# Optimization experiments

Hardware: AMD Instinct MI355X
Metric: run time of the kernel (lower is better)

Reference implementation:

```python
import jax, jax.numpy as jnp
import numpy as np

B, T, D, H, W = 2, 16, 64, 64, 64
E, EXP = 4, 2
TWO_D = 2 * D
HID = EXP * TWO_D


def layernorm(x, g, b, eps=1e-5):
    m = x.mean(-1, keepdims=True)
    v = ((x - m) ** 2).mean(-1, keepdims=True)
    return (x - m) / jnp.sqrt(v + eps) * g + b


def pscan(A, X):
    # h_t = A_t * h_{t-1} + X_t, scanned over axis=1 (time); complex-valued.
    def comb(c1, c2):
        a1, x1 = c1
        a2, x2 = c2
        return a1 * a2, a2 * x1 + x2
    return jax.lax.associative_scan(comb, (A, X), axis=1)[1]


def setup_inputs() -> dict:
    key = jax.random.key(0)
    ks = jax.random.split(key, 24)
    def s(i, shape, scale=0.05):
        return jax.random.normal(ks[i], shape, jnp.float32) * scale
    return {
        "x_re": jax.random.normal(ks[0], (B, T, D, H, W), jnp.float32),
        "x_im": jax.random.normal(ks[1], (B, T, D, H, W), jnp.float32),
        "dt": jax.random.uniform(ks[2], (T,), jnp.float32, 0.5, 1.5),
        "ln_s_g": jnp.ones((TWO_D,), jnp.float32),
        "ln_s_b": jnp.zeros((TWO_D,), jnp.float32),
        "conv_w": s(3, (TWO_D, TWO_D, 3, 3)),
        "conv_b": jnp.zeros((TWO_D,), jnp.float32),
        "ln_t_g": jnp.ones((TWO_D,), jnp.float32),
        "ln_t_b": jnp.zeros((TWO_D,), jnp.float32),
        "enc_re": s(4, (D, D)), "enc_im": s(5, (D, D)),
        "dec_re": s(6, (D, D)), "dec_im": s(7, (D, D)),
        "alpha": s(8, (D,), 0.5), "omega": s(9, (D,), 1.0),
        "wg": s(10, (TWO_D, D)), "bg": jnp.zeros((D,), jnp.float32),
        "p_re": s(11, (D, D)), "p_im": s(12, (D, D)),
        "w_drift": s(13, (TWO_D, D)), "b_drift": jnp.zeros((D,), jnp.float32),
        "w_router": s(14, (TWO_D, E)),
        "w1": s(15, (E, TWO_D, HID)), "w2": s(16, (E, HID, TWO_D)),
        "noise_scale": jnp.float32(0.01),
    }


def reference(x_re, x_im, dt, ln_s_g, ln_s_b, conv_w, conv_b, ln_t_g, ln_t_b,
              enc_re, enc_im, dec_re, dec_im, alpha, omega, wg, bg,
              p_re, p_im, w_drift, b_drift, w_router, w1, w2, noise_scale):
    x = x_re + 1j * x_im  # [B,T,D,H,W] complex64
    N = B * T
    xf = x.reshape(N, D, H, W)
    xr = jnp.concatenate([xf.real, xf.imag], axis=1)  # [N,2D,H,W]
    # spatial LayerNorm over channels
    xn = layernorm(xr.transpose(0, 2, 3, 1), ln_s_g, ln_s_b).transpose(0, 3, 1, 2)
    # Clifford spatial conv (standard 3x3 same-conv on stacked re/im channels)
    xs = jax.lax.conv_general_dilated(xn, conv_w, (1, 1), 'SAME',
                                      dimension_numbers=('NCHW', 'OIHW', 'NCHW'))
    xs = xs + conv_b[None, :, None, None]
    x_sc = xs[:, :D] + 1j * xs[:, D:]            # [N,D,H,W]
    x5 = x_sc.reshape(B, T, D, H, W)              # complex
    # basis encode: complex channel mixing
    enc = enc_re + 1j * enc_im
    u_t = jnp.einsum('bthwd,de->bthwe', x5.transpose(0, 1, 3, 4, 2), enc)  # [B,T,H,W,D]

    # ---- global flux tracker (pscan #1) ----
    x_mean = x5.mean(axis=(-2, -1))               # [B,T,D] complex
    feat = jnp.concatenate([x_mean.real, x_mean.imag], axis=-1)  # [B,T,2D]
    gate = jax.nn.sigmoid(feat @ wg + bg)         # [B,T,D]
    flux_A = gate.astype(jnp.complex64)
    flux_X = (1.0 - gate) * x_mean
    flux_state = pscan(flux_A, flux_X)            # [B,T,D]
    flux_out = flux_state @ (p_re + 1j * p_im)    # [B,T,D]
    drift_in = jnp.concatenate([flux_out.real, flux_out.imag], axis=-1)
    drift = drift_in @ w_drift + b_drift          # [B,T,D] (dead code in source; kept for fidelity)
    drift_c = drift[..., : D // 2] + 1j * drift[..., D // 2:]
    del drift_c

    # ---- temporal propagation (pscan #2) ----
    dt_e = dt.reshape(1, T, 1, 1, 1)              # broadcast (B,T,H,W,1)
    lam = -jax.nn.softplus(alpha) + 1j * omega    # [D]
    decay = jnp.exp(lam * dt_e)                   # [1,T,1,1,D]
    forcing = (decay - 1.0) / lam                 # ZOH forcing operator
    u_scaled = u_t * forcing                      # [B,T,H,W,D]
    decay_full = jnp.broadcast_to(decay, (B, T, H, W, D))
    A_time = decay_full.transpose(0, 2, 3, 1, 4).reshape(B * H * W, T, D)
    X_time = u_scaled.transpose(0, 2, 3, 1, 4).reshape(B * H * W, T, D)
    Y = pscan(A_time, X_time)
    u_out = Y.reshape(B, H, W, T, D).transpose(0, 3, 1, 2, 4)  # [B,T,H,W,D]
    # deterministic surrogate for the SDE stochastic term (state-proportional)
    u_out = u_out + noise_scale * jnp.sqrt(dt_e) * u_out
    dec = dec_re + 1j * dec_im
    x_out = jnp.einsum('bthwd,de->bthwe', u_out, dec)  # decode
    x_out = x_out.transpose(0, 1, 4, 2, 3).reshape(N, D, H, W)
    xo_r = jnp.concatenate([x_out.real, x_out.imag], axis=1)
    xo_n = layernorm(xo_r.transpose(0, 2, 3, 1), ln_t_g, ln_t_b)  # [N,H,W,2D]

    # ---- MoE FFN over pixels (soft mixture of experts) ----
    gates = jax.nn.softmax(xo_n @ w_router, axis=-1)  # [N,H,W,E]
    acc = jnp.zeros_like(xo_n)
    for e in range(E):
        h = jax.nn.gelu(xo_n @ w1[e])
        acc = acc + gates[..., e:e + 1] * (h @ w2[e])
    delta = acc[..., :D] + 1j * acc[..., D:]          # [N,H,W,D]
    delta = delta.transpose(0, 3, 1, 2).reshape(B, T, D, H, W)
    return x + delta
```

## Files before the change

kernel.cpp:

```cpp
#include <hip/hip_runtime.h>
#include <hip/hip_bf16.h>

#define BB 2
#define TT 16
#define DD 64
#define HH 64
#define WW 64
#define NPIX 131072


typedef unsigned short u16;
typedef unsigned int u32;
typedef __attribute__((ext_vector_type(8))) short bf16x8;
typedef __attribute__((ext_vector_type(4))) float f32x4;

union U16x8 { uint4 u4; uint2 u2[2]; u16 h[8]; bf16x8 v; };

__device__ __forceinline__ float us2f(u16 u) {
  union { u32 i; float f; } c; c.i = ((u32)u) << 16; return c.f;
}
__device__ __forceinline__ u16 f2us(float f) {
  u32 x = __float_as_uint(f);
  u32 r = x + 0x7fffu + ((x >> 16) & 1u);
  return (u16)(r >> 16);
}

__global__ __launch_bounds__(256) void k0_prep(
    const float* __restrict__ conv_w,
    const float* __restrict__ enc_re, const float* __restrict__ enc_im,
    const float* __restrict__ dec_re, const float* __restrict__ dec_im,
    const float* __restrict__ w1, const float* __restrict__ w2,
    u16* __restrict__ mencs, u16* __restrict__ mdecs,
    u16* __restrict__ wcs, u16* __restrict__ w1s, u16* __restrict__ w2s) {
  int idx = blockIdx.x * 256 + threadIdx.x;
  if (idx < 65536) {
    int m = idx >> 15;
    int z = idx & 32767;
    int s = z >> 14;
    int q = z & 16383;
    int j = q & 7, lane = (q >> 3) & 63, ks = (q >> 9) & 3, nt = (q >> 11) & 7;
    int k = ks * 32 + (lane >> 4) * 8 + j;
    int n = nt * 16 + (lane & 15);
    const float* mre = m ? dec_re : enc_re;
    const float* mim = m ? dec_im : enc_im;
    float v;
    if (k < 64) v = (n < 64) ?  mre[k * 64 + n]        : mim[k * 64 + n - 64];
    else        v = (n < 64) ? -mim[(k - 64) * 64 + n] : mre[(k - 64) * 64 + n - 64];
    u16 hi = f2us(v);
    u16 val = s ? f2us(v - us2f(hi)) : hi;
    u16* dst = m ? mdecs : mencs;
    dst[((nt * 8 + s * 4 + ks) * 64 + lane) * 8 + j] = val;
  } else if (idx < 212992) {
    int z = idx - 65536;
    int j = z & 7, lane = (z >> 3) & 63, ks = (z >> 9) & 3, nt = (z >> 11) & 7, tap = z >> 14;
    int ic = ks * 32 + (lane >> 4) * 8 + j;
    int oc = nt * 16 + (lane & 15);
    wcs[z] = f2us(conv_w[(oc * 128 + ic) * 9 + tap]);
  } else if (idx < 344064) {
    int z = idx - 212992;
    int j = z & 7, lane = (z >> 3) & 63, ks = (z >> 9) & 3, nt = (z >> 11) & 15, e = z >> 15;
    int k = ks * 32 + (lane >> 4) * 8 + j;
    int nn = nt * 16 + (lane & 15);
    w1s[z] = f2us(w1[e * 32768 + k * 256 + nn]);
  } else if (idx < 475136) {
    int z = idx - 344064;
    int j = z & 7, lane = (z >> 3) & 63, ks = (z >> 9) & 7, nt = (z >> 12) & 7, e = z >> 15;
    int k = ks * 32 + (lane >> 4) * 8 + j;
    int nn = nt * 16 + (lane & 15);
    w2s[z] = f2us(w2[e * 32768 + k * 128 + nn]);
  }
}

__global__ __launch_bounds__(256) void k1_spatial_ln(
    const float* __restrict__ x_re, const float* __restrict__ x_im,
    const float* __restrict__ g, const float* __restrict__ b,
    u16* __restrict__ xn) {
  __shared__ float tile[64 * 129];
  __shared__ float meanA[64], rstdA[64];
  int n = blockIdx.x >> 6, h = blockIdx.x & 63;
  int tid = threadIdx.x;
  for (int k = 0; k < 32; ++k) {
    int flat = tid + k * 256;
    int c = flat >> 6, w = flat & 63;
    float v = (c < 64) ? x_re[n * 262144 + c * 4096 + h * 64 + w]
                       : x_im[n * 262144 + (c - 64) * 4096 + h * 64 + w];
    tile[w * 129 + c] = v;
  }
  __syncthreads();
  int p = tid >> 2, q = tid & 3;
  float s = 0.f, ss = 0.f;
  for (int c = q * 32; c < q * 32 + 32; ++c) {
    float v = tile[p * 129 + c];
    s += v; ss += v * v;
  }
  s += __shfl_xor(s, 1); ss += __shfl_xor(ss, 1);
  s += __shfl_xor(s, 2); ss += __shfl_xor(ss, 2);
  if (q == 0) {
    float m = s * (1.0f / 128.0f);
    float var = ss * (1.0f / 128.0f) - m * m;
    meanA[p] = m; rstdA[p] = rsqrtf(var + 1e-5f);
  }
  __syncthreads();
  int rowbase = (n * 4096 + h * 64) * 128;
  for (int k = 0; k < 32; ++k) {
    int flat = tid + k * 256;
    int pp = flat >> 7, c = flat & 127;
    float v = (tile[pp * 129 + c] - meanA[pp]) * rstdA[pp] * g[c] + b[c];
    xn[rowbase + flat] = f2us(v);
  }
}

__global__ __launch_bounds__(256) void k2_mfma(
    const u16* __restrict__ xn, const u16* __restrict__ wcs,
    const float* __restrict__ conv_b, u16* __restrict__ xs) {
  __shared__ __align__(16) u16 Xs[3 * 66 * 132];
  int tid = threadIdx.x;
  int wave = tid >> 6, lane = tid & 63;
  int quad = lane >> 4, am = lane & 15;
  int n = blockIdx.x >> 6, h = blockIdx.x & 63;

  for (int dh = 0; dh < 3; ++dh) {
    int hs = h + dh - 1;
    bool valid = (hs >= 0) && (hs < 64);
    const u16* src = xn + (n * 4096 + hs * 64) * 128;
    for (int c = 0; c < 4; ++c) {
      int f8 = tid + c * 256;
      int px = f8 >> 4, ch = (f8 & 15) * 8;
      uint2 lo = make_uint2(0, 0), hi = make_uint2(0, 0);
      if (valid) {
        const uint2* s2 = (const uint2*)(src + px * 128 + ch);
        lo = s2[0]; hi = s2[1];
      }
      u16* dst = Xs + (dh * 66 + px + 1) * 132 + ch;
      *(uint2*)dst = lo;
      *(uint2*)(dst + 4) = hi;
    }
  }
  for (int z = tid; z < 792; z += 256) {
    int dh = z / 264, r = z % 264;
    int px = (r < 132) ? 0 : 65;
    Xs[(dh * 66 + px) * 132 + (r % 132)] = 0;
  }
  __syncthreads();

  f32x4 acc[8];
#pragma unroll
  for (int nt = 0; nt < 8; ++nt) {
    float bv = conv_b[nt * 16 + am];
    acc[nt] = (f32x4){bv, bv, bv, bv};
  }
  int mt = wave;
  for (int tap = 0; tap < 9; ++tap) {
    int dh = tap / 3, dw = tap % 3;
    const u16* arow = Xs + (dh * 66 + mt * 16 + am + dw) * 132 + quad * 8;
    bf16x8 a[4];
#pragma unroll
    for (int ks = 0; ks < 4; ++ks) {
      U16x8 t;
      t.u2[0] = *(const uint2*)(arow + ks * 32);
      t.u2[1] = *(const uint2*)(arow + ks * 32 + 4);
      a[ks] = t.v;
    }
    const uint4* wp = (const uint4*)wcs + tap * 2048 + lane;
    uint4 wb[4];
#pragma unroll
    for (int ks = 0; ks < 4; ++ks) wb[ks] = wp[ks * 64];
    for (int nt = 0; nt < 8; ++nt) {
      uint4 wn[4];
      if (nt < 7) {
#pragma unroll
        for (int ks = 0; ks < 4; ++ks) wn[ks] = wp[((nt + 1) * 4 + ks) * 64];
      }
#pragma unroll
      for (int ks = 0; ks < 4; ++ks) {
        U16x8 bf; bf.u4 = wb[ks];
        acc[nt] = __builtin_amdgcn_mfma_f32_16x16x32_bf16(a[ks], bf.v, acc[nt], 0, 0, 0);
      }
      if (nt < 7) {
#pragma unroll
        for (int ks = 0; ks < 4; ++ks) wb[ks] = wn[ks];
      }
    }
  }
  int rowg = n * 4096 + h * 64;
#pragma unroll
  for (int nt = 0; nt < 8; ++nt)
#pragma unroll
    for (int r = 0; r < 4; ++r)
      xs[(rowg + mt * 16 + quad * 4 + r) * 128 + nt * 16 + am] = f2us(acc[nt][r]);
}

__global__ __launch_bounds__(256) void k3_mfma(
    u16* X, const u16* __restrict__ ms) {
  int tid = threadIdx.x;
  int wave = tid >> 6, lane = tid & 63;
  int quad = lane >> 4, am = lane & 15;
  int rowbase = blockIdx.x * 128 + wave * 32;

  bf16x8 ax[2][4];
#pragma unroll
  for (int mt = 0; mt < 2; ++mt) {
    const uint4* ar = (const uint4*)(X + (rowbase + mt * 16 + am) * 128 + quad * 8);
#pragma unroll
    for (int ks = 0; ks < 4; ++ks) { U16x8 t; t.u4 = ar[ks * 4]; ax[mt][ks] = t.v; }
  }
  const uint4* mp = (const uint4*)ms + lane;
  uint4 wb[8];
#pragma unroll
  for (int kk = 0; kk < 8; ++kk) wb[kk] = mp[kk * 64];
  for (int nt = 0; nt < 8; ++nt) {
    uint4 wn[8];
    if (nt < 7) {
#pragma unroll
      for (int kk = 0; kk < 8; ++kk) wn[kk] = mp[((nt + 1) * 8 + kk) * 64];
    }
    f32x4 ca = (f32x4){0.f, 0.f, 0.f, 0.f};
    f32x4 cb = (f32x4){0.f, 0.f, 0.f, 0.f};
#pragma unroll
    for (int kk = 0; kk < 8; ++kk) {
      U16x8 bf; bf.u4 = wb[kk];
      ca = __builtin_amdgcn_mfma_f32_16x16x32_bf16(ax[0][kk & 3], bf.v, ca, 0, 0, 0);
      cb = __builtin_amdgcn_mfma_f32_16x16x32_bf16(ax[1][kk & 3], bf.v, cb, 0, 0, 0);
    }
#pragma unroll
    for (int r = 0; r < 4; ++r) {
      X[(rowbase + quad * 4 + r) * 128 + nt * 16 + am]      = f2us(ca[r]);
      X[(rowbase + 16 + quad * 4 + r) * 128 + nt * 16 + am] = f2us(cb[r]);
    }
    if (nt < 7) {
#pragma unroll
      for (int kk = 0; kk < 8; ++kk) wb[kk] = wn[kk];
    }
  }
}

__global__ __launch_bounds__(256) void k_scan(
    u16* __restrict__ u, const float* __restrict__ dt,
    const float* __restrict__ alpha, const float* __restrict__ omega,
    const float* __restrict__ ns_p) {
  int flat = blockIdx.x * 256 + threadIdx.x;
  int d = flat & 63;
  int hw = (flat >> 6) & 4095;
  int b = flat >> 18;
  float a = alpha[d];
  float sp = (a > 20.f) ? a : log1pf(expf(a));
  float lr = -sp, li = omega[d];
  float inv_l2 = 1.0f / (lr * lr + li * li);
  float ns = ns_p[0];
  float yr = 0.f, yi = 0.f;
  const int stride = 4096 * 128;
  int base0 = b * 16 * stride + hw * 128 + d;
  for (int t = 0; t < 16; ++t) {
    float dtv = dt[t];
    float er = expf(lr * dtv);
    float ang = li * dtv;
    float dr = er * cosf(ang), di = er * sinf(ang);
    float fr = ((dr - 1.f) * lr + di * li) * inv_l2;
    float fi = (di * lr - (dr - 1.f) * li) * inv_l2;
    int idx = base0 + t * stride;
    float ur = us2f(u[idx]), ui = us2f(u[idx + 64]);
    float usr = ur * fr - ui * fi;
    float usi = ur * fi + ui * fr;
    float nyr = dr * yr - di * yi + usr;
    float nyi = dr * yi + di * yr + usi;
    yr = nyr; yi = nyi;
    float sc = 1.0f + ns * sqrtf(dtv);
    u[idx] = f2us(yr * sc);
    u[idx + 64] = f2us(yi * sc);
  }
}

__global__ __launch_bounds__(256) void k4_mfma(
    const u16* __restrict__ U, const u16* __restrict__ ms,
    const float* __restrict__ g, const float* __restrict__ bb,
    u16* __restrict__ xo) {
  int tid = threadIdx.x;
  int wave = tid >> 6, lane = tid & 63;
  int quad = lane >> 4, am = lane & 15;
  int rowbase = blockIdx.x * 128 + wave * 32;

  bf16x8 ax[2][4];
#pragma unroll
  for (int mt = 0; mt < 2; ++mt) {
    const uint4* ar = (const uint4*)(U + (rowbase + mt * 16 + am) * 128 + quad * 8);
#pragma unroll
    for (int ks = 0; ks < 4; ++ks) { U16x8 t; t.u4 = ar[ks * 4]; ax[mt][ks] = t.v; }
  }
  float gv[8], bv[8];
#pragma unroll
  for (int nt = 0; nt < 8; ++nt) { gv[nt] = g[nt * 16 + am]; bv[nt] = bb[nt * 16 + am]; }

  const uint4* mp = (const uint4*)ms + lane;
  f32x4 acc[2][8];
#pragma unroll
  for (int mt = 0; mt < 2; ++mt)
#pragma unroll
    for (int nt = 0; nt < 8; ++nt) acc[mt][nt] = (f32x4){0.f, 0.f, 0.f, 0.f};

  uint4 wb[8];
#pragma unroll
  for (int kk = 0; kk < 8; ++kk) wb[kk] = mp[kk * 64];
  for (int nt = 0; nt < 8; ++nt) {
    uint4 wn[8];
    if (nt < 7) {
#pragma unroll
      for (int kk = 0; kk < 8; ++kk) wn[kk] = mp[((nt + 1) * 8 + kk) * 64];
    }
#pragma unroll
    for (int kk = 0; kk < 8; ++kk) {
      U16x8 bf; bf.u4 = wb[kk];
      acc[0][nt] = __builtin_amdgcn_mfma_f32_16x16x32_bf16(ax[0][kk & 3], bf.v, acc[0][nt], 0, 0, 0);
      acc[1][nt] = __builtin_amdgcn_mfma_f32_16x16x32_bf16(ax[1][kk & 3], bf.v, acc[1][nt], 0, 0, 0);
    }
    if (nt < 7) {
#pragma unroll
      for (int kk = 0; kk < 8; ++kk) wb[kk] = wn[kk];
    }
  }

#pragma unroll
  for (int mt = 0; mt < 2; ++mt) {
#pragma unroll
    for (int r = 0; r < 4; ++r) {
      float s = 0.f, ss = 0.f;
#pragma unroll
      for (int nt = 0; nt < 8; ++nt) { float v = acc[mt][nt][r]; s += v; ss += v * v; }
      s += __shfl_xor(s, 1); ss += __shfl_xor(ss, 1);
      s += __shfl_xor(s, 2); ss += __shfl_xor(ss, 2);
      s += __shfl_xor(s, 4); ss += __shfl_xor(ss, 4);
      s += __shfl_xor(s, 8); ss += __shfl_xor(ss, 8);
      float m = s * (1.0f / 128.0f);
      float var = ss * (1.0f / 128.0f) - m * m;
      float rstd = rsqrtf(var + 1e-5f);
      u16* xop = xo + (rowbase + mt * 16 + quad * 4 + r) * 128 + am;
#pragma unroll
      for (int nt = 0; nt < 8; ++nt)
        xop[nt * 16] = f2us((acc[mt][nt][r] - m) * rstd * gv[nt] + bv[nt]);
    }
  }
}

__global__ __launch_bounds__(256) void k5_mfma(
    const u16* __restrict__ xo, const u16* __restrict__ w1s,
    const u16* __restrict__ w2s, const float* __restrict__ w_router,
    const float* __restrict__ x_re, const float* __restrict__ x_im,
    u16* __restrict__ out) {
  __shared__ __align__(16) u16 Hs[128 * 280];
  __shared__ float gate_s[128 * 4];
  int tid = threadIdx.x;
  int wave = tid >> 6, lane = tid & 63;
  int quad = lane >> 4, am = lane & 15;
  int rowbase = blockIdx.x * 128 + wave * 32;

  for (int pp = 0; pp < 2; ++pp) {
    int pxl = wave * 32 + pp * 16 + am;
    const uint4* xr = (const uint4*)(xo + (blockIdx.x * 128 + pxl) * 128);
    float acc = 0.f;
    for (int c8 = 0; c8 < 16; ++c8) {
      U16x8 t; t.u4 = xr[c8];
#pragma unroll
      for (int j = 0; j < 8; ++j)
        acc += us2f(t.h[j]) * w_router[(c8 * 8 + j) * 4 + quad];
    }
    float mx = fmaxf(acc, __shfl_xor(acc, 16));
    mx = fmaxf(mx, __shfl_xor(mx, 32));
    float ex = __expf(acc - mx);
    float sm = ex + __shfl_xor(ex, 16);
    sm += __shfl_xor(sm, 32);
    gate_s[pxl * 4 + quad] = ex / sm;
  }

  bf16x8 ax[2][4];
#pragma unroll
  for (int mt = 0; mt < 2; ++mt) {
    const uint4* ar = (const uint4*)(xo + (rowbase + mt * 16 + am) * 128 + quad * 8);
#pragma unroll
    for (int ks = 0; ks < 4; ++ks) { U16x8 t; t.u4 = ar[ks * 4]; ax[mt][ks] = t.v; }
  }

  f32x4 c2[2][8];
#pragma unroll
  for (int mt = 0; mt < 2; ++mt)
#pragma unroll
    for (int nt = 0; nt < 8; ++nt) c2[mt][nt] = (f32x4){0.f, 0.f, 0.f, 0.f};

  const float GA2 = 2.3022085f, GB2 = 0.10294348f;

  for (int e = 0; e < 4; ++e) {
    const uint4* w1p = (const uint4*)w1s + e * 4096 + lane;
    uint4 wb[4];
#pragma unroll
    for (int ks = 0; ks < 4; ++ks) wb[ks] = w1p[ks * 64];
    for (int nt = 0; nt < 16; ++nt) {
      uint4 wn[4];
      if (nt < 15) {
#pragma unroll
        for (int ks = 0; ks < 4; ++ks) wn[ks] = w1p[((nt + 1) * 4 + ks) * 64];
      }
      f32x4 c1a = (f32x4){0.f, 0.f, 0.f, 0.f};
      f32x4 c1b = (f32x4){0.f, 0.f, 0.f, 0.f};
#pragma unroll
      for (int ks = 0; ks < 4; ++ks) {
        U16x8 bf; bf.u4 = wb[ks];
        c1a = __builtin_amdgcn_mfma_f32_16x16x32_bf16(ax[0][ks], bf.v, c1a, 0, 0, 0);
        c1b = __builtin_amdgcn_mfma_f32_16x16x32_bf16(ax[1][ks], bf.v, c1b, 0, 0, 0);
      }
#pragma unroll
      for (int r = 0; r < 4; ++r) {
        float v = c1a[r];
        float gv0 = gate_s[(wave * 32 + quad * 4 + r) * 4 + e] * v;
        float rc = __builtin_amdgcn_rcpf(
            1.0f + __builtin_amdgcn_exp2f(v * (GA2 + GB2 * v * v)));
        Hs[(wave * 32 + quad * 4 + r) * 280 + nt * 16 + am] = f2us(gv0 - gv0 * rc);
        v = c1b[r];
        float gv1 = gate_s[(wave * 32 + 16 + quad * 4 + r) * 4 + e] * v;
        rc = __builtin_amdgcn_rcpf(
            1.0f + __builtin_amdgcn_exp2f(v * (GA2 + GB2 * v * v)));
        Hs[(wave * 32 + 16 + quad * 4 + r) * 280 + nt * 16 + am] = f2us(gv1 - gv1 * rc);
      }
      if (nt < 15) {
#pragma unroll
        for (int ks = 0; ks < 4; ++ks) wb[ks] = wn[ks];
      }
    }
    const uint4* w2p = (const uint4*)w2s + e * 4096 + lane;
    uint4 wb2[8];
#pragma unroll
    for (int nt = 0; nt < 8; ++nt) wb2[nt] = w2p[(nt * 8) * 64];
    for (int ks = 0; ks < 8; ++ks) {
      uint4 wn2[8];
      if (ks < 7) {
#pragma unroll
        for (int nt = 0; nt < 8; ++nt) wn2[nt] = w2p[(nt * 8 + ks + 1) * 64];
      }
      U16x8 a2[2];
#pragma unroll
      for (int mt = 0; mt < 2; ++mt)
        a2[mt].u4 = *(const uint4*)(Hs + (wave * 32 + mt * 16 + am) * 280 + ks * 32 + quad * 8);
#pragma unroll
      for (int nt = 0; nt < 8; ++nt) {
        U16x8 bf; bf.u4 = wb2[nt];
        c2[0][nt] = __builtin_amdgcn_mfma_f32_16x16x32_bf16(a2[0].v, bf.v, c2[0][nt], 0, 0, 0);
        c2[1][nt] = __builtin_amdgcn_mfma_f32_16x16x32_bf16(a2[1].v, bf.v, c2[1][nt], 0, 0, 0);
      }
      if (ks < 7) {
#pragma unroll
        for (int nt = 0; nt < 8; ++nt) wb2[nt] = wn2[nt];
      }
    }
  }

  __syncthreads();
  float* Os = (float*)Hs;
#pragma unroll
  for (int nt = 0; nt < 4; ++nt)
#pragma unroll
    for (int mt = 0; mt < 2; ++mt)
#pragma unroll
      for (int r = 0; r < 4; ++r) {
        int pxl = wave * 32 + mt * 16 + quad * 4 + r;
        Os[(nt * 16 + am) * 129 + pxl]      = c2[mt][nt][r];
        Os[(64 + nt * 16 + am) * 129 + pxl] = c2[mt][nt + 4][r];
      }
  __syncthreads();
  int nb  = (blockIdx.x * 128) >> 12;
  int hw0 = (blockIdx.x * 128) & 4095;
#pragma unroll
  for (int k = 0; k < 32; ++k) {
    int flat = tid + k * 256;
    int d = flat >> 7, px = flat & 127;
    int gidx = (nb * 64 + d) * 4096 + hw0 + px;
    float rr = x_re[gidx] + Os[d * 129 + px];
    float ii = x_im[gidx] + Os[(64 + d) * 129 + px];
    ((u32*)out)[gidx] = (u32)f2us(ii) | ((u32)f2us(rr) << 16);
  }
}

extern "C" void kernel_launch(void* const* d_in, const int* in_sizes, int n_in,
                              void* d_out, int out_size, void* d_ws, size_t ws_size,
                              hipStream_t stream) {
  const float* x_re     = (const float*)d_in[0];
  const float* x_im     = (const float*)d_in[1];
  const float* dt       = (const float*)d_in[2];
  const float* ln_s_g   = (const float*)d_in[3];
  const float* ln_s_b   = (const float*)d_in[4];
  const float* conv_w   = (const float*)d_in[5];
  const float* conv_b   = (const float*)d_in[6];
  const float* ln_t_g   = (const float*)d_in[7];
  const float* ln_t_b   = (const float*)d_in[8];
  const float* enc_re   = (const float*)d_in[9];
  const float* enc_im   = (const float*)d_in[10];
  const float* dec_re   = (const float*)d_in[11];
  const float* dec_im   = (const float*)d_in[12];
  const float* alpha    = (const float*)d_in[13];
  const float* omega    = (const float*)d_in[14];
  const float* w_router = (const float*)d_in[21];
  const float* w1       = (const float*)d_in[22];
  const float* w2       = (const float*)d_in[23];
  const float* ns       = (const float*)d_in[24];

  u16*   buf   = (u16*)d_ws;
  u16*   mencs = (u16*)((char*)d_ws + 33554432);
  u16*   mdecs = mencs + 32768;
  u16*   wcs   = mdecs + 32768;
  u16*   w1s   = wcs + 147456;
  u16*   w2s   = w1s + 131072;
  u16*   outf  = (u16*)d_out;

  k0_prep<<<1856, 256, 0, stream>>>(conv_w, enc_re, enc_im, dec_re, dec_im,
                                    w1, w2, mencs, mdecs, wcs, w1s, w2s);
  k1_spatial_ln<<<2048, 256, 0, stream>>>(x_re, x_im, ln_s_g, ln_s_b, buf);
  k2_mfma<<<2048, 256, 0, stream>>>(buf, wcs, conv_b, outf);
  k3_mfma<<<1024, 256, 0, stream>>>(outf, mencs);
  k_scan<<<2048, 256, 0, stream>>>(outf, dt, alpha, omega, ns);
  k4_mfma<<<1024, 256, 0, stream>>>(outf, mdecs, ln_t_g, ln_t_b, buf);
  k5_mfma<<<1024, 256, 0, stream>>>(buf, w1s, w2s, w_router, x_re, x_im, outf);
}
```

Before: 458.0 us.

## Fuse conv and encoder GEMM kernels, process two rows per block

The 3x3 conv kernel now processes two image rows per block and reuses each loaded weight fragment for both rows. The conv result is staged in shared memory as bf16 and immediately multiplied by the encoder matrix, which removes the separate k3 kernel and its global round trip. This costs more LDS and more accumulator registers per thread, halves the grid, and adds an extra barrier between the stages.

```diff
diff --git a/kernel.cpp b/kernel.cpp
--- a/kernel.cpp
+++ b/kernel.cpp
@@ -112,15 +112,17 @@
 
 __global__ __launch_bounds__(256) void k2_mfma(
     const u16* __restrict__ xn, const u16* __restrict__ wcs,
-    const float* __restrict__ conv_b, u16* __restrict__ xs) {
-  __shared__ __align__(16) u16 Xs[3 * 66 * 132];
+    const float* __restrict__ conv_b, const u16* __restrict__ ms,
+    u16* __restrict__ xs) {
+  __shared__ __align__(16) u16 Xs[4 * 66 * 132];
   int tid = threadIdx.x;
   int wave = tid >> 6, lane = tid & 63;
   int quad = lane >> 4, am = lane & 15;
-  int n = blockIdx.x >> 6, h = blockIdx.x & 63;
-
-  for (int dh = 0; dh < 3; ++dh) {
-    int hs = h + dh - 1;
+  int n = blockIdx.x >> 5, hp = blockIdx.x & 31;
+  int h0 = hp * 2;
+
+  for (int dh = 0; dh < 4; ++dh) {
+    int hs = h0 + dh - 1;
     bool valid = (hs >= 0) && (hs < 64);
     const u16* src = xn + (n * 4096 + hs * 64) * 128;
     for (int c = 0; c < 4; ++c) {
@@ -136,30 +138,33 @@
       *(uint2*)(dst + 4) = hi;
     }
   }
-  for (int z = tid; z < 792; z += 256) {
+  for (int z = tid; z < 1056; z += 256) {
     int dh = z / 264, r = z % 264;
     int px = (r < 132) ? 0 : 65;
     Xs[(dh * 66 + px) * 132 + (r % 132)] = 0;
   }
   __syncthreads();
 
-  f32x4 acc[8];
+  f32x4 acc[2][8];
 #pragma unroll
   for (int nt = 0; nt < 8; ++nt) {
     float bv = conv_b[nt * 16 + am];
-    acc[nt] = (f32x4){bv, bv, bv, bv};
-  }
-  int mt = wave;
+    acc[0][nt] = (f32x4){bv, bv, bv, bv};
+    acc[1][nt] = (f32x4){bv, bv, bv, bv};
+  }
   for (int tap = 0; tap < 9; ++tap) {
     int dh = tap / 3, dw = tap % 3;
-    const u16* arow = Xs + (dh * 66 + mt * 16 + am + dw) * 132 + quad * 8;
-    bf16x8 a[4];
-#pragma unroll
-    for (int ks = 0; ks < 4; ++ks) {
-      U16x8 t;
-      t.u2[0] = *(const uint2*)(arow + ks * 32);
-      t.u2[1] = *(const uint2*)(arow + ks * 32 + 4);
-      a[ks] = t.v;
+    bf16x8 a[2][4];
+#pragma unroll
+    for (int mt = 0; mt < 2; ++mt) {
+      const u16* arow = Xs + ((dh + mt) * 66 + wave * 16 + am + dw) * 132 + quad * 8;
+#pragma unroll
+      for (int ks = 0; ks < 4; ++ks) {
+        U16x8 t;
+        t.u2[0] = *(const uint2*)(arow + ks * 32);
+        t.u2[1] = *(const uint2*)(arow + ks * 32 + 4);
+        a[mt][ks] = t.v;
+      }
     }
     const uint4* wp = (const uint4*)wcs + tap * 2048 + lane;
     uint4 wb[4];
@@ -174,7 +179,8 @@
 #pragma unroll
       for (int ks = 0; ks < 4; ++ks) {
         U16x8 bf; bf.u4 = wb[ks];
-        acc[nt] = __builtin_amdgcn_mfma_f32_16x16x32_bf16(a[ks], bf.v, acc[nt], 0, 0, 0);
+        acc[0][nt] = __builtin_amdgcn_mfma_f32_16x16x32_bf16(a[0][ks], bf.v, acc[0][nt], 0, 0, 0);
+        acc[1][nt] = __builtin_amdgcn_mfma_f32_16x16x32_bf16(a[1][ks], bf.v, acc[1][nt], 0, 0, 0);
       }
       if (nt < 7) {
 #pragma unroll
@@ -182,32 +188,34 @@
       }
     }
   }
-  int rowg = n * 4096 + h * 64;
-#pragma unroll
-  for (int nt = 0; nt < 8; ++nt)
-#pragma unroll
-    for (int r = 0; r < 4; ++r)
-      xs[(rowg + mt * 16 + quad * 4 + r) * 128 + nt * 16 + am] = f2us(acc[nt][r]);
-}
-
-__global__ __launch_bounds__(256) void k3_mfma(
-    u16* X, const u16* __restrict__ ms) {
-  int tid = threadIdx.x;
-  int wave = tid >> 6, lane = tid & 63;
-  int quad = lane >> 4, am = lane & 15;
-  int rowbase = blockIdx.x * 128 + wave * 32;
-
-  bf16x8 ax[2][4];
+
+  __syncthreads();
+  u16* Cs = Xs;
+#pragma unroll
+  for (int mt = 0; mt < 2; ++mt)
+#pragma unroll
+    for (int nt = 0; nt < 8; ++nt)
+#pragma unroll
+      for (int r = 0; r < 4; ++r)
+        Cs[(mt * 64 + wave * 16 + quad * 4 + r) * 136 + nt * 16 + am] =
+            f2us(acc[mt][nt][r]);
+  __syncthreads();
+
+  bf16x8 a2[2][4];
 #pragma unroll
   for (int mt = 0; mt < 2; ++mt) {
-    const uint4* ar = (const uint4*)(X + (rowbase + mt * 16 + am) * 128 + quad * 8);
-#pragma unroll
-    for (int ks = 0; ks < 4; ++ks) { U16x8 t; t.u4 = ar[ks * 4]; ax[mt][ks] = t.v; }
+    const u16* crow = Cs + (mt * 64 + wave * 16 + am) * 136;
+#pragma unroll
+    for (int ks = 0; ks < 4; ++ks) {
+      U16x8 t; t.u4 = *(const uint4*)(crow + ks * 32 + quad * 8);
+      a2[mt][ks] = t.v;
+    }
   }
   const uint4* mp = (const uint4*)ms + lane;
   uint4 wb[8];
 #pragma unroll
   for (int kk = 0; kk < 8; ++kk) wb[kk] = mp[kk * 64];
+  int rowg0 = n * 4096 + h0 * 64 + wave * 16;
   for (int nt = 0; nt < 8; ++nt) {
     uint4 wn[8];
     if (nt < 7) {
@@ -219,13 +227,13 @@
 #pragma unroll
     for (int kk = 0; kk < 8; ++kk) {
       U16x8 bf; bf.u4 = wb[kk];
-      ca = __builtin_amdgcn_mfma_f32_16x16x32_bf16(ax[0][kk & 3], bf.v, ca, 0, 0, 0);
-      cb = __builtin_amdgcn_mfma_f32_16x16x32_bf16(ax[1][kk & 3], bf.v, cb, 0, 0, 0);
+      ca = __builtin_amdgcn_mfma_f32_16x16x32_bf16(a2[0][kk & 3], bf.v, ca, 0, 0, 0);
+      cb = __builtin_amdgcn_mfma_f32_16x16x32_bf16(a2[1][kk & 3], bf.v, cb, 0, 0, 0);
     }
 #pragma unroll
     for (int r = 0; r < 4; ++r) {
-      X[(rowbase + quad * 4 + r) * 128 + nt * 16 + am]      = f2us(ca[r]);
-      X[(rowbase + 16 + quad * 4 + r) * 128 + nt * 16 + am] = f2us(cb[r]);
+      xs[(rowg0 + quad * 4 + r) * 128 + nt * 16 + am]      = f2us(ca[r]);
+      xs[(rowg0 + 64 + quad * 4 + r) * 128 + nt * 16 + am] = f2us(cb[r]);
     }
     if (nt < 7) {
 #pragma unroll
@@ -510,8 +518,7 @@
   k0_prep<<<1856, 256, 0, stream>>>(conv_w, enc_re, enc_im, dec_re, dec_im,
                                     w1, w2, mencs, mdecs, wcs, w1s, w2s);
   k1_spatial_ln<<<2048, 256, 0, stream>>>(x_re, x_im, ln_s_g, ln_s_b, buf);
-  k2_mfma<<<2048, 256, 0, stream>>>(buf, wcs, conv_b, outf);
-  k3_mfma<<<1024, 256, 0, stream>>>(outf, mencs);
+  k2_mfma<<<1024, 256, 0, stream>>>(buf, wcs, conv_b, mencs, outf);
   k_scan<<<2048, 256, 0, stream>>>(outf, dt, alpha, omega, ns);
   k4_mfma<<<1024, 256, 0, stream>>>(outf, mdecs, ln_t_g, ln_t_b, buf);
   k5_mfma<<<1024, 256, 0, stream>>>(buf, w1s, w2s, w_router, x_re, x_im, outf);
```

Result: no change. 465.2 us (+1.6%).

## Fuse encoder complex matmul into conv kernel epilogue via LDS staging

Applied to the files above, without the earlier changes.

The separate k3 encoder matmul kernel is removed. The conv output tile is staged in shared memory, reloaded as MFMA A-fragments, and multiplied by the encoder matrix inside k2 before writing to global memory. This drops a full global write and read of the intermediate bf16 activation plus one kernel launch. In exchange, k2 does more work per block and loads encoder weights without prefetch, which may add register pressure and latency.

```diff
diff --git a/kernel.cpp b/kernel.cpp
--- a/kernel.cpp
+++ b/kernel.cpp
@@ -112,7 +112,8 @@
 
 __global__ __launch_bounds__(256) void k2_mfma(
     const u16* __restrict__ xn, const u16* __restrict__ wcs,
-    const float* __restrict__ conv_b, u16* __restrict__ xs) {
+    const float* __restrict__ conv_b, const u16* __restrict__ ms,
+    u16* __restrict__ xs) {
   __shared__ __align__(16) u16 Xs[3 * 66 * 132];
   int tid = threadIdx.x;
   int wave = tid >> 6, lane = tid & 63;
@@ -182,54 +183,41 @@
       }
     }
   }
-  int rowg = n * 4096 + h * 64;
+
+  __syncthreads();
+  u16* Cs = Xs;
 #pragma unroll
   for (int nt = 0; nt < 8; ++nt)
 #pragma unroll
     for (int r = 0; r < 4; ++r)
-      xs[(rowg + mt * 16 + quad * 4 + r) * 128 + nt * 16 + am] = f2us(acc[nt][r]);
-}
-
-__global__ __launch_bounds__(256) void k3_mfma(
-    u16* X, const u16* __restrict__ ms) {
-  int tid = threadIdx.x;
-  int wave = tid >> 6, lane = tid & 63;
-  int quad = lane >> 4, am = lane & 15;
-  int rowbase = blockIdx.x * 128 + wave * 32;
-
-  bf16x8 ax[2][4];
-#pragma unroll
-  for (int mt = 0; mt < 2; ++mt) {
-    const uint4* ar = (const uint4*)(X + (rowbase + mt * 16 + am) * 128 + quad * 8);
-#pragma unroll
-    for (int ks = 0; ks < 4; ++ks) { U16x8 t; t.u4 = ar[ks * 4]; ax[mt][ks] = t.v; }
+      Cs[(wave * 16 + quad * 4 + r) * 136 + nt * 16 + am] = f2us(acc[nt][r]);
+  __syncthreads();
+
+  bf16x8 a2[4];
+  {
+    const u16* crow = Cs + (wave * 16 + am) * 136;
+#pragma unroll
+    for (int ks = 0; ks < 4; ++ks) {
+      U16x8 t; t.u4 = *(const uint4*)(crow + ks * 32 + quad * 8);
+      a2[ks] = t.v;
+    }
   }
   const uint4* mp = (const uint4*)ms + lane;
-  uint4 wb[8];
-#pragma unroll
-  for (int kk = 0; kk < 8; ++kk) wb[kk] = mp[kk * 64];
-  for (int nt = 0; nt < 8; ++nt) {
-    uint4 wn[8];
-    if (nt < 7) {
-#pragma unroll
-      for (int kk = 0; kk < 8; ++kk) wn[kk] = mp[((nt + 1) * 8 + kk) * 64];
-    }
+  int rowg = n * 4096 + h * 64 + wave * 16;
+  for (int p = 0; p < 4; ++p) {
     f32x4 ca = (f32x4){0.f, 0.f, 0.f, 0.f};
     f32x4 cb = (f32x4){0.f, 0.f, 0.f, 0.f};
 #pragma unroll
     for (int kk = 0; kk < 8; ++kk) {
-      U16x8 bf; bf.u4 = wb[kk];
-      ca = __builtin_amdgcn_mfma_f32_16x16x32_bf16(ax[0][kk & 3], bf.v, ca, 0, 0, 0);
-      cb = __builtin_amdgcn_mfma_f32_16x16x32_bf16(ax[1][kk & 3], bf.v, cb, 0, 0, 0);
+      U16x8 b0; b0.u4 = mp[((2 * p) * 8 + kk) * 64];
+      U16x8 b1; b1.u4 = mp[((2 * p + 1) * 8 + kk) * 64];
+      ca = __builtin_amdgcn_mfma_f32_16x16x32_bf16(a2[kk & 3], b0.v, ca, 0, 0, 0);
+      cb = __builtin_amdgcn_mfma_f32_16x16x32_bf16(a2[kk & 3], b1.v, cb, 0, 0, 0);
     }
 #pragma unroll
     for (int r = 0; r < 4; ++r) {
-      X[(rowbase + quad * 4 + r) * 128 + nt * 16 + am]      = f2us(ca[r]);
-      X[(rowbase + 16 + quad * 4 + r) * 128 + nt * 16 + am] = f2us(cb[r]);
-    }
-    if (nt < 7) {
-#pragma unroll
-      for (int kk = 0; kk < 8; ++kk) wb[kk] = wn[kk];
+      xs[(rowg + quad * 4 + r) * 128 + (2 * p) * 16 + am]     = f2us(ca[r]);
+      xs[(rowg + quad * 4 + r) * 128 + (2 * p + 1) * 16 + am] = f2us(cb[r]);
     }
   }
 }
@@ -510,8 +498,7 @@
   k0_prep<<<1856, 256, 0, stream>>>(conv_w, enc_re, enc_im, dec_re, dec_im,
                                     w1, w2, mencs, mdecs, wcs, w1s, w2s);
   k1_spatial_ln<<<2048, 256, 0, stream>>>(x_re, x_im, ln_s_g, ln_s_b, buf);
-  k2_mfma<<<2048, 256, 0, stream>>>(buf, wcs, conv_b, outf);
-  k3_mfma<<<1024, 256, 0, stream>>>(outf, mencs);
+  k2_mfma<<<2048, 256, 0, stream>>>(buf, wcs, conv_b, mencs, outf);
   k_scan<<<2048, 256, 0, stream>>>(outf, dt, alpha, omega, ns);
   k4_mfma<<<1024, 256, 0, stream>>>(outf, mdecs, ln_t_g, ln_t_b, buf);
   k5_mfma<<<1024, 256, 0, stream>>>(buf, w1s, w2s, w_router, x_re, x_im, outf);
```

Result: no change. 456.8 us (-0.3%).
